# Kernel tuning notes

Hardware: AMD Instinct MI355X
Metric: run time of the kernel (lower is better)

## Reference

```python
import jax, jax.numpy as jnp
import numpy as np

EPS = 1e-08

def setup_inputs() -> dict:
    key = jax.random.key(0)
    k1, k2, k3, k4 = jax.random.split(key, 4)
    B, N, IN, OUT, WF = 16, 4096, 512, 512, 512
    x = jax.random.normal(k1, (B, N, IN), dtype=jnp.float32)
    w = jax.random.normal(k2, (B, WF), dtype=jnp.float32)
    # kaiming-normal-like init for the main weight
    weight = jax.random.normal(k3, (OUT, IN), dtype=jnp.float32) * np.sqrt(2.0 / IN)
    bias = jnp.zeros((OUT,), dtype=jnp.float32)
    A_w = jax.random.normal(k4, (IN, WF), dtype=jnp.float32) * np.sqrt(1.0 / WF)
    A_b = jnp.zeros((IN,), dtype=jnp.float32)
    return {"x": x, "w": w, "weight": weight, "bias": bias, "A_w": A_w, "A_b": A_b}

def reference(x, w, weight, bias, A_w, A_b):
    # style -> per-input-channel scale: (B, in)
    s = w @ A_w.T + A_b
    # modulate: (B, out, in)
    wm = weight[None, :, :] * s[:, None, :]
    # demodulate: rsqrt over in-dim
    norm = jax.lax.rsqrt(EPS + jnp.sum(wm * wm, axis=2, keepdims=True))
    wd = wm * norm
    # batched matmul: (B, N, in) x (B, out, in) -> (B, N, out)
    out = jnp.einsum('bni,boi->bno', x, wd) + bias
    return jax.nn.relu(out)
```

## Files before the change

kernel.cpp:

```cpp
#include <hip/hip_runtime.h>
#include <hip/hip_bf16.h>

#define B_    16
#define M_    4096
#define K_    512
#define O_    512

#define BM 128
#define BN 128
#define BK 32

typedef float f32x4 __attribute__((ext_vector_type(4)));
typedef short bf16x8 __attribute__((ext_vector_type(8)));
typedef unsigned short u16x8 __attribute__((ext_vector_type(8)));

__device__ __forceinline__ int chunk_off(int row, int kq) {
    return (row * 4 + (kq ^ ((row >> 1) & 3))) * 8;
}

__global__ void style_kernel(const float* __restrict__ w, const float* __restrict__ A_w,
                             const float* __restrict__ A_b, float* __restrict__ s) {
    int b = blockIdx.x;
    int i = blockIdx.y * 64 + threadIdx.x;
    __shared__ float wsh[512];
    for (int j = threadIdx.x; j < 512; j += 64) wsh[j] = w[b * 512 + j];
    __syncthreads();
    const float* arow = A_w + (size_t)i * 512;
    float acc = 0.f;
    #pragma unroll 4
    for (int f = 0; f < 512; f += 4) {
        float4 a = *(const float4*)(arow + f);
        acc += a.x * wsh[f] + a.y * wsh[f + 1] + a.z * wsh[f + 2] + a.w * wsh[f + 3];
    }
    s[b * 512 + i] = acc + A_b[i];
}

__global__ void demod_kernel(const float* __restrict__ weight, const float* __restrict__ s,
                             unsigned short* __restrict__ wd) {
    int gw = blockIdx.x * 4 + (threadIdx.x >> 6);
    int lane = threadIdx.x & 63;
    int b = gw >> 9;
    int o = gw & 511;
    const float* wrow = weight + (size_t)o * 512;
    const float* srow = s + b * 512;
    float vals[8];
    float ss = 0.f;
    #pragma unroll
    for (int j = 0; j < 8; j++) {
        int i = lane + j * 64;
        float v = wrow[i] * srow[i];
        vals[j] = v;
        ss += v * v;
    }
    #pragma unroll
    for (int off = 32; off; off >>= 1) ss += __shfl_xor(ss, off);
    float nrm = rsqrtf(1e-8f + ss);
    unsigned short* drow = wd + ((size_t)b * 512 + o) * 512;
    #pragma unroll
    for (int j = 0; j < 8; j++) {
        int i = lane + j * 64;
        unsigned int u = __builtin_bit_cast(unsigned int, vals[j] * nrm);
        u += 0x7fffu + ((u >> 16) & 1u);
        drow[i] = (unsigned short)(u >> 16);
    }
}

__global__ __launch_bounds__(256, 3) void gemm_kernel(const float* __restrict__ x,
                                                      const unsigned short* __restrict__ wd,
                                                      const float* __restrict__ bias,
                                                      float* __restrict__ out) {
    __shared__ unsigned short sA[2][BM * BK];
    __shared__ unsigned short sB[2][BN * BK];

    int g = blockIdx.x;
    int xcd = g & 7;
    int grp = g >> 3;
    int nblk = grp & 3;
    int mb = xcd * 64 + (grp >> 2);
    const int b  = mb >> 5;
    const int m0 = (mb & 31) * BM;
    const int n0 = nblk * BN;

    const float* xb = x + (size_t)b * M_ * K_;
    const unsigned short* wdb = wd + (size_t)b * O_ * K_;

    const int t = threadIdx.x;
    const int w = t >> 6;
    const int l = t & 63;
    const int wave_row = (w >> 1) * 64;
    const int wave_col = (w & 1) * 64;
    const int lrow  = l & 15;
    const int kq_l  = l >> 4;

    int offA[4], offB[4];
    #pragma unroll
    for (int mi = 0; mi < 4; mi++)
        offA[mi] = chunk_off(wave_row + mi * 16 + lrow, kq_l);
    #pragma unroll
    for (int ni = 0; ni < 4; ni++)
        offB[ni] = chunk_off(wave_col + ni * 16 + lrow, kq_l);

    const int ar = t >> 1;
    const int akq0 = (t & 1) * 2;
    const float* abase = xb + (size_t)(m0 + ar) * K_ + akq0 * 8;

    int bchunk[2], brow[2], bkq[2];
    #pragma unroll
    for (int j = 0; j < 2; j++) {
        int c = w * 128 + j * 64 + l;
        brow[j] = c >> 2;
        bkq[j] = (c & 3) ^ ((brow[j] >> 1) & 3);
        bchunk[j] = c;
    }

    f32x4 acc[4][4] = {};
    f32x4 areg[4];

    #pragma unroll
    for (int j = 0; j < 2; j++) {
        __builtin_amdgcn_global_load_lds(
            (const __attribute__((address_space(1))) unsigned int*)(wdb + (size_t)(n0 + brow[j]) * K_ + bkq[j] * 8),
            (__attribute__((address_space(3))) unsigned int*)(&sB[0][bchunk[j] * 8]),
            16, 0, 0);
    }
    #pragma unroll
    for (int j = 0; j < 4; j++) areg[j] = *(const f32x4*)(abase + j * 4);
    #pragma unroll
    for (int j = 0; j < 2; j++) {
        union { __hip_bfloat162 h[4]; u16x8 v; } cv;
        cv.h[0] = __float22bfloat162_rn(float2{areg[2*j][0], areg[2*j][1]});
        cv.h[1] = __float22bfloat162_rn(float2{areg[2*j][2], areg[2*j][3]});
        cv.h[2] = __float22bfloat162_rn(float2{areg[2*j+1][0], areg[2*j+1][1]});
        cv.h[3] = __float22bfloat162_rn(float2{areg[2*j+1][2], areg[2*j+1][3]});
        *(u16x8*)(&sA[0][chunk_off(ar, akq0 + j)]) = cv.v;
    }
    __syncthreads();

    int cur = 0;
    #pragma unroll 2
    for (int kk = 0; kk < K_; kk += BK) {
        int nxt = cur ^ 1;
        bool pf = (kk + BK) < K_;
        if (pf) {
            #pragma unroll
            for (int j = 0; j < 2; j++) {
                __builtin_amdgcn_global_load_lds(
                    (const __attribute__((address_space(1))) unsigned int*)(wdb + (size_t)(n0 + brow[j]) * K_ + kk + BK + bkq[j] * 8),
                    (__attribute__((address_space(3))) unsigned int*)(&sB[nxt][bchunk[j] * 8]),
                    16, 0, 0);
            }
            #pragma unroll
            for (int j = 0; j < 4; j++) areg[j] = *(const f32x4*)(abase + kk + BK + j * 4);
        }

        bf16x8 af[4], bfr[4];
        #pragma unroll
        for (int mi = 0; mi < 4; mi++) af[mi] = *(const bf16x8*)(&sA[cur][offA[mi]]);
        #pragma unroll
        for (int ni = 0; ni < 4; ni++) bfr[ni] = *(const bf16x8*)(&sB[cur][offB[ni]]);
        #pragma unroll
        for (int mi = 0; mi < 4; mi++)
            #pragma unroll
            for (int ni = 0; ni < 4; ni++)
                acc[mi][ni] = __builtin_amdgcn_mfma_f32_16x16x32_bf16(af[mi], bfr[ni], acc[mi][ni], 0, 0, 0);

        if (pf) {
            #pragma unroll
            for (int j = 0; j < 2; j++) {
                union { __hip_bfloat162 h[4]; u16x8 v; } cv;
                cv.h[0] = __float22bfloat162_rn(float2{areg[2*j][0], areg[2*j][1]});
                cv.h[1] = __float22bfloat162_rn(float2{areg[2*j][2], areg[2*j][3]});
                cv.h[2] = __float22bfloat162_rn(float2{areg[2*j+1][0], areg[2*j+1][1]});
                cv.h[3] = __float22bfloat162_rn(float2{areg[2*j+1][2], areg[2*j+1][3]});
                *(u16x8*)(&sA[nxt][chunk_off(ar, akq0 + j)]) = cv.v;
            }
        }
        __syncthreads();
        cur = nxt;
    }

    const int col_l = l & 15;
    const int row_q = (l >> 4) * 4;
    #pragma unroll
    for (int ni = 0; ni < 4; ni++) {
        int o = n0 + wave_col + ni * 16 + col_l;
        float bv = bias[o];
        #pragma unroll
        for (int mi = 0; mi < 4; mi++) {
            int mrow = m0 + wave_row + mi * 16 + row_q;
            #pragma unroll
            for (int r = 0; r < 4; r++) {
                float v = acc[mi][ni][r] + bv;
                out[((size_t)b * M_ + mrow + r) * O_ + o] = v > 0.f ? v : 0.f;
            }
        }
    }
}

extern "C" void kernel_launch(void* const* d_in, const int* in_sizes, int n_in,
                              void* d_out, int out_size, void* d_ws, size_t ws_size,
                              hipStream_t stream) {
    const float* x      = (const float*)d_in[0];
    const float* w      = (const float*)d_in[1];
    const float* weight = (const float*)d_in[2];
    const float* bias   = (const float*)d_in[3];
    const float* A_w    = (const float*)d_in[4];
    const float* A_b    = (const float*)d_in[5];
    float* out = (float*)d_out;

    unsigned short* wd = (unsigned short*)d_ws;
    float* s = (float*)((char*)d_ws + (size_t)B_ * O_ * K_ * sizeof(unsigned short));

    style_kernel<<<dim3(B_, 8), 64, 0, stream>>>(w, A_w, A_b, s);
    demod_kernel<<<(B_ * O_) / 4, 256, 0, stream>>>(weight, s, wd);
    gemm_kernel<<<2048, 256, 0, stream>>>(x, wd, bias, out);
}
```

Measured before the change: 308.1 us.

## Deepen GEMM pipeline to triple-buffered LDS with two-tile-ahead prefetch

Moves the GEMM main loop from double to triple-buffered LDS and issues global loads two k-tiles ahead, alternating two register sets for the fp32 A tile. Plain __syncthreads is replaced by explicit s_waitcnt vmcnt(6) plus a barrier, so the next tile's loads can stay in flight while the current tile is computed. The aim is to hide global memory latency better. In exchange it uses more LDS (48KB per block, which may limit residency at 3 blocks per CU) and more registers, and correctness depends on the hand-counted vmcnt value.

```diff
diff --git a/kernel.cpp b/kernel.cpp
--- a/kernel.cpp
+++ b/kernel.cpp
@@ -9,6 +9,7 @@
 #define BM 128
 #define BN 128
 #define BK 32
+#define NT (K_ / BK)
 
 typedef float f32x4 __attribute__((ext_vector_type(4)));
 typedef short bf16x8 __attribute__((ext_vector_type(8)));
@@ -65,12 +66,63 @@
     }
 }
 
+
+#define ISSUE_B(tile, buf)                                                              \
+    _Pragma("unroll")                                                                   \
+    for (int j = 0; j < 2; j++) {                                                       \
+        __builtin_amdgcn_global_load_lds(                                               \
+            (const __attribute__((address_space(1))) unsigned int*)(                    \
+                wdb + (size_t)(n0 + brow[j]) * K_ + (tile) * BK + bkq[j] * 8),          \
+            (__attribute__((address_space(3))) unsigned int*)(&sB[buf][bchunk[j] * 8]), \
+            16, 0, 0);                                                                  \
+    }
+
+#define LOAD_A(tile, regs)                                                              \
+    _Pragma("unroll")                                                                   \
+    for (int j = 0; j < 4; j++) regs[j] = *(const f32x4*)(abase + (tile) * BK + j * 4);
+
+#define CVT_A(regs, buf)                                                                \
+    _Pragma("unroll")                                                                   \
+    for (int j = 0; j < 2; j++) {                                                       \
+        union { __hip_bfloat162 h[4]; u16x8 v; } cv;                                    \
+        cv.h[0] = __float22bfloat162_rn(float2{regs[2*j][0], regs[2*j][1]});            \
+        cv.h[1] = __float22bfloat162_rn(float2{regs[2*j][2], regs[2*j][3]});            \
+        cv.h[2] = __float22bfloat162_rn(float2{regs[2*j+1][0], regs[2*j+1][1]});        \
+        cv.h[3] = __float22bfloat162_rn(float2{regs[2*j+1][2], regs[2*j+1][3]});        \
+        *(u16x8*)(&sA[buf][chunk_off(ar, akq0 + j)]) = cv.v;                            \
+    }
+
+#define COMPUTE(buf)                                                                    \
+    {                                                                                   \
+        bf16x8 af[4], bfr[4];                                                           \
+        _Pragma("unroll")                                                               \
+        for (int mi = 0; mi < 4; mi++) af[mi] = *(const bf16x8*)(&sA[buf][offA[mi]]);   \
+        _Pragma("unroll")                                                               \
+        for (int ni = 0; ni < 4; ni++) bfr[ni] = *(const bf16x8*)(&sB[buf][offB[ni]]);  \
+        _Pragma("unroll")                                                               \
+        for (int mi = 0; mi < 4; mi++)                                                  \
+            _Pragma("unroll")                                                           \
+            for (int ni = 0; ni < 4; ni++)                                              \
+                acc[mi][ni] = __builtin_amdgcn_mfma_f32_16x16x32_bf16(                  \
+                    af[mi], bfr[ni], acc[mi][ni], 0, 0, 0);                             \
+    }
+
+#define FENCE6() do {                                                                   \
+    asm volatile("s_waitcnt vmcnt(6) lgkmcnt(0)" ::: "memory");                         \
+    __builtin_amdgcn_s_barrier();                                                       \
+} while (0)
+
+#define FENCE0() do {                                                                   \
+    asm volatile("s_waitcnt vmcnt(0) lgkmcnt(0)" ::: "memory");                         \
+    __builtin_amdgcn_s_barrier();                                                       \
+} while (0)
+
 __global__ __launch_bounds__(256, 3) void gemm_kernel(const float* __restrict__ x,
                                                       const unsigned short* __restrict__ wd,
                                                       const float* __restrict__ bias,
                                                       float* __restrict__ out) {
-    __shared__ unsigned short sA[2][BM * BK];
-    __shared__ unsigned short sB[2][BN * BK];
+    __shared__ unsigned short sA[3][BM * BK];
+    __shared__ unsigned short sB[3][BN * BK];
 
     int g = blockIdx.x;
     int xcd = g & 7;
@@ -114,69 +166,29 @@
     }
 
     f32x4 acc[4][4] = {};
-    f32x4 areg[4];
-
-    #pragma unroll
-    for (int j = 0; j < 2; j++) {
-        __builtin_amdgcn_global_load_lds(
-            (const __attribute__((address_space(1))) unsigned int*)(wdb + (size_t)(n0 + brow[j]) * K_ + bkq[j] * 8),
-            (__attribute__((address_space(3))) unsigned int*)(&sB[0][bchunk[j] * 8]),
-            16, 0, 0);
-    }
-    #pragma unroll
-    for (int j = 0; j < 4; j++) areg[j] = *(const f32x4*)(abase + j * 4);
-    #pragma unroll
-    for (int j = 0; j < 2; j++) {
-        union { __hip_bfloat162 h[4]; u16x8 v; } cv;
-        cv.h[0] = __float22bfloat162_rn(float2{areg[2*j][0], areg[2*j][1]});
-        cv.h[1] = __float22bfloat162_rn(float2{areg[2*j][2], areg[2*j][3]});
-        cv.h[2] = __float22bfloat162_rn(float2{areg[2*j+1][0], areg[2*j+1][1]});
-        cv.h[3] = __float22bfloat162_rn(float2{areg[2*j+1][2], areg[2*j+1][3]});
-        *(u16x8*)(&sA[0][chunk_off(ar, akq0 + j)]) = cv.v;
-    }
-    __syncthreads();
-
-    int cur = 0;
-    #pragma unroll 2
-    for (int kk = 0; kk < K_; kk += BK) {
-        int nxt = cur ^ 1;
-        bool pf = (kk + BK) < K_;
-        if (pf) {
-            #pragma unroll
-            for (int j = 0; j < 2; j++) {
-                __builtin_amdgcn_global_load_lds(
-                    (const __attribute__((address_space(1))) unsigned int*)(wdb + (size_t)(n0 + brow[j]) * K_ + kk + BK + bkq[j] * 8),
-                    (__attribute__((address_space(3))) unsigned int*)(&sB[nxt][bchunk[j] * 8]),
-                    16, 0, 0);
-            }
-            #pragma unroll
-            for (int j = 0; j < 4; j++) areg[j] = *(const f32x4*)(abase + kk + BK + j * 4);
+    f32x4 areg0[4], areg1[4];
+
+    ISSUE_B(0, 0);
+    LOAD_A(0, areg0);
+    asm volatile("" ::: "memory");
+    ISSUE_B(1, 1);
+    LOAD_A(1, areg1);
+    CVT_A(areg0, 0);
+    FENCE6();
+
+    #pragma unroll
+    for (int k = 0; k < NT; k++) {
+        if (k + 2 < NT) {
+            ISSUE_B(k + 2, (k + 2) % 3);
+            if ((k & 1) == 0) { LOAD_A(k + 2, areg0); } else { LOAD_A(k + 2, areg1); }
         }
 
-        bf16x8 af[4], bfr[4];
-        #pragma unroll
-        for (int mi = 0; mi < 4; mi++) af[mi] = *(const bf16x8*)(&sA[cur][offA[mi]]);
-        #pragma unroll
-        for (int ni = 0; ni < 4; ni++) bfr[ni] = *(const bf16x8*)(&sB[cur][offB[ni]]);
-        #pragma unroll
-        for (int mi = 0; mi < 4; mi++)
-            #pragma unroll
-            for (int ni = 0; ni < 4; ni++)
-                acc[mi][ni] = __builtin_amdgcn_mfma_f32_16x16x32_bf16(af[mi], bfr[ni], acc[mi][ni], 0, 0, 0);
-
-        if (pf) {
-            #pragma unroll
-            for (int j = 0; j < 2; j++) {
-                union { __hip_bfloat162 h[4]; u16x8 v; } cv;
-                cv.h[0] = __float22bfloat162_rn(float2{areg[2*j][0], areg[2*j][1]});
-                cv.h[1] = __float22bfloat162_rn(float2{areg[2*j][2], areg[2*j][3]});
-                cv.h[2] = __float22bfloat162_rn(float2{areg[2*j+1][0], areg[2*j+1][1]});
-                cv.h[3] = __float22bfloat162_rn(float2{areg[2*j+1][2], areg[2*j+1][3]});
-                *(u16x8*)(&sA[nxt][chunk_off(ar, akq0 + j)]) = cv.v;
-            }
+        COMPUTE(k % 3);
+
+        if (k + 1 < NT) {
+            if ((k & 1) == 0) { CVT_A(areg1, (k + 1) % 3); } else { CVT_A(areg0, (k + 1) % 3); }
+            if (k + 2 < NT) { FENCE6(); } else { FENCE0(); }
         }
-        __syncthreads();
-        cur = nxt;
     }
 
     const int col_l = l & 15;
```

Measured after the change: 340.9 us. 10.6% more time.

## Restructure GEMM: full-K A tile in LDS, B fragments loaded directly from pre-swizzled layout

Applied to the files above, without the earlier changes.

The demod kernel now writes the modulated weights in an MFMA-fragment-ordered layout, so the GEMM can load B fragments straight from global memory into registers with double buffering and no LDS staging. Each GEMM block covers 64 rows and all 512 output columns, loading the whole 64x512 bf16 A tile into LDS once. This removes the per-k-step barriers and uses setprio around the MFMA burst. The style kernel is rebuilt to compute 16 outputs per block from LDS-staged tiles. In exchange, register pressure is higher (128 accumulator vectors plus 16 B fragments per wave), occupancy is capped at 2 blocks, and there are fewer blocks.

```diff
diff --git a/kernel.cpp b/kernel.cpp
--- a/kernel.cpp
+++ b/kernel.cpp
@@ -6,192 +6,155 @@
 #define K_    512
 #define O_    512
 
-#define BM 128
-#define BN 128
-#define BK 32
+#define BM 64
+#define NT 16
 
 typedef float f32x4 __attribute__((ext_vector_type(4)));
 typedef short bf16x8 __attribute__((ext_vector_type(8)));
 typedef unsigned short u16x8 __attribute__((ext_vector_type(8)));
 
-__device__ __forceinline__ int chunk_off(int row, int kq) {
-    return (row * 4 + (kq ^ ((row >> 1) & 3))) * 8;
-}
-
 __global__ void style_kernel(const float* __restrict__ w, const float* __restrict__ A_w,
                              const float* __restrict__ A_b, float* __restrict__ s) {
-    int b = blockIdx.x;
-    int i = blockIdx.y * 64 + threadIdx.x;
-    __shared__ float wsh[512];
-    for (int j = threadIdx.x; j < 512; j += 64) wsh[j] = w[b * 512 + j];
+    __shared__ float wsh[16][516];
+    __shared__ float ash[16][516];
+    int t = threadIdx.x;
+    for (int idx = t; idx < 2048; idx += 256) {
+        int row = idx >> 7, q = (idx & 127) * 4;
+        *(float4*)&wsh[row][q] = *(const float4*)&w[row * 512 + q];
+    }
+    int i0 = blockIdx.x * 16;
+    for (int idx = t; idx < 2048; idx += 256) {
+        int row = idx >> 7, q = (idx & 127) * 4;
+        *(float4*)&ash[row][q] = *(const float4*)&A_w[(size_t)(i0 + row) * 512 + q];
+    }
     __syncthreads();
-    const float* arow = A_w + (size_t)i * 512;
+    int b = t >> 4, il = t & 15;
     float acc = 0.f;
-    #pragma unroll 4
+    #pragma unroll 8
     for (int f = 0; f < 512; f += 4) {
-        float4 a = *(const float4*)(arow + f);
-        acc += a.x * wsh[f] + a.y * wsh[f + 1] + a.z * wsh[f + 2] + a.w * wsh[f + 3];
+        float4 wa = *(const float4*)&wsh[b][f];
+        float4 aa = *(const float4*)&ash[il][f];
+        acc += wa.x * aa.x + wa.y * aa.y + wa.z * aa.z + wa.w * aa.w;
     }
-    s[b * 512 + i] = acc + A_b[i];
+    s[b * 512 + i0 + il] = acc + A_b[i0 + il];
 }
 
 __global__ void demod_kernel(const float* __restrict__ weight, const float* __restrict__ s,
-                             unsigned short* __restrict__ wd) {
+                             unsigned short* __restrict__ wd2) {
     int gw = blockIdx.x * 4 + (threadIdx.x >> 6);
     int lane = threadIdx.x & 63;
     int b = gw >> 9;
     int o = gw & 511;
     const float* wrow = weight + (size_t)o * 512;
     const float* srow = s + b * 512;
+    int k0 = lane * 8;
+    f32x4 w0 = *(const f32x4*)(wrow + k0);
+    f32x4 w1 = *(const f32x4*)(wrow + k0 + 4);
+    f32x4 s0 = *(const f32x4*)(srow + k0);
+    f32x4 s1 = *(const f32x4*)(srow + k0 + 4);
     float vals[8];
     float ss = 0.f;
     #pragma unroll
-    for (int j = 0; j < 8; j++) {
-        int i = lane + j * 64;
-        float v = wrow[i] * srow[i];
-        vals[j] = v;
-        ss += v * v;
-    }
+    for (int j = 0; j < 4; j++) { float v = w0[j] * s0[j]; vals[j] = v; ss += v * v; }
+    #pragma unroll
+    for (int j = 0; j < 4; j++) { float v = w1[j] * s1[j]; vals[4 + j] = v; ss += v * v; }
     #pragma unroll
     for (int off = 32; off; off >>= 1) ss += __shfl_xor(ss, off);
     float nrm = rsqrtf(1e-8f + ss);
-    unsigned short* drow = wd + ((size_t)b * 512 + o) * 512;
+    int ks = lane >> 2, kq = lane & 3;
+    size_t base = (((((size_t)b * 16 + ks) * 32 + (o >> 4)) * 4 + kq) * 16 + (o & 15)) * 8;
+    u16x8 pack;
     #pragma unroll
     for (int j = 0; j < 8; j++) {
-        int i = lane + j * 64;
         unsigned int u = __builtin_bit_cast(unsigned int, vals[j] * nrm);
         u += 0x7fffu + ((u >> 16) & 1u);
-        drow[i] = (unsigned short)(u >> 16);
+        pack[j] = (unsigned short)(u >> 16);
     }
+    *(u16x8*)(wd2 + base) = pack;
 }
 
-__global__ __launch_bounds__(256, 3) void gemm_kernel(const float* __restrict__ x,
-                                                      const unsigned short* __restrict__ wd,
+__global__ __launch_bounds__(256, 2) void gemm_kernel(const float* __restrict__ x,
+                                                      const unsigned short* __restrict__ wd2,
                                                       const float* __restrict__ bias,
                                                       float* __restrict__ out) {
-    __shared__ unsigned short sA[2][BM * BK];
-    __shared__ unsigned short sB[2][BN * BK];
+    __shared__ unsigned short sA[BM * 64 * 8];
 
     int g = blockIdx.x;
     int xcd = g & 7;
-    int grp = g >> 3;
-    int nblk = grp & 3;
-    int mb = xcd * 64 + (grp >> 2);
-    const int b  = mb >> 5;
-    const int m0 = (mb & 31) * BM;
-    const int n0 = nblk * BN;
-
-    const float* xb = x + (size_t)b * M_ * K_;
-    const unsigned short* wdb = wd + (size_t)b * O_ * K_;
+    int r = g >> 3;
+    const int b  = xcd * 2 + (r >> 6);
+    const int m0 = (r & 63) * BM;
 
     const int t = threadIdx.x;
     const int w = t >> 6;
     const int l = t & 63;
-    const int wave_row = (w >> 1) * 64;
-    const int wave_col = (w & 1) * 64;
-    const int lrow  = l & 15;
-    const int kq_l  = l >> 4;
 
-    int offA[4], offB[4];
+    const float* xb = x + ((size_t)b * M_ + m0) * K_;
     #pragma unroll
-    for (int mi = 0; mi < 4; mi++)
-        offA[mi] = chunk_off(wave_row + mi * 16 + lrow, kq_l);
-    #pragma unroll
-    for (int ni = 0; ni < 4; ni++)
-        offB[ni] = chunk_off(wave_col + ni * 16 + lrow, kq_l);
-
-    const int ar = t >> 1;
-    const int akq0 = (t & 1) * 2;
-    const float* abase = xb + (size_t)(m0 + ar) * K_ + akq0 * 8;
-
-    int bchunk[2], brow[2], bkq[2];
-    #pragma unroll
-    for (int j = 0; j < 2; j++) {
-        int c = w * 128 + j * 64 + l;
-        brow[j] = c >> 2;
-        bkq[j] = (c & 3) ^ ((brow[j] >> 1) & 3);
-        bchunk[j] = c;
-    }
-
-    f32x4 acc[4][4] = {};
-    f32x4 areg[4];
-
-    #pragma unroll
-    for (int j = 0; j < 2; j++) {
-        __builtin_amdgcn_global_load_lds(
-            (const __attribute__((address_space(1))) unsigned int*)(wdb + (size_t)(n0 + brow[j]) * K_ + bkq[j] * 8),
-            (__attribute__((address_space(3))) unsigned int*)(&sB[0][bchunk[j] * 8]),
-            16, 0, 0);
-    }
-    #pragma unroll
-    for (int j = 0; j < 4; j++) areg[j] = *(const f32x4*)(abase + j * 4);
-    #pragma unroll
-    for (int j = 0; j < 2; j++) {
-        union { __hip_bfloat162 h[4]; u16x8 v; } cv;
-        cv.h[0] = __float22bfloat162_rn(float2{areg[2*j][0], areg[2*j][1]});
-        cv.h[1] = __float22bfloat162_rn(float2{areg[2*j][2], areg[2*j][3]});
-        cv.h[2] = __float22bfloat162_rn(float2{areg[2*j+1][0], areg[2*j+1][1]});
-        cv.h[3] = __float22bfloat162_rn(float2{areg[2*j+1][2], areg[2*j+1][3]});
-        *(u16x8*)(&sA[0][chunk_off(ar, akq0 + j)]) = cv.v;
+    for (int rr = 0; rr < 16; rr++) {
+        int row = rr * 4 + w;
+        const float* src = xb + (size_t)row * K_ + l * 8;
+        f32x4 u = *(const f32x4*)src;
+        f32x4 v = *(const f32x4*)(src + 4);
+        union { __hip_bfloat162 h[4]; u16x8 vv; } cv;
+        cv.h[0] = __float22bfloat162_rn(float2{u[0], u[1]});
+        cv.h[1] = __float22bfloat162_rn(float2{u[2], u[3]});
+        cv.h[2] = __float22bfloat162_rn(float2{v[0], v[1]});
+        cv.h[3] = __float22bfloat162_rn(float2{v[2], v[3]});
+        int chunk = row * 64 + (l & ~7) + ((l ^ row) & 7);
+        *(u16x8*)(&sA[chunk * 8]) = cv.vv;
     }
     __syncthreads();
 
-    int cur = 0;
-    #pragma unroll 2
-    for (int kk = 0; kk < K_; kk += BK) {
-        int nxt = cur ^ 1;
-        bool pf = (kk + BK) < K_;
-        if (pf) {
+    const unsigned short* wb = wd2 + (size_t)b * 262144 + (size_t)(w * 8) * 512 + (size_t)l * 8;
+
+    const int rowl = l & 15;
+    const int kqv  = l >> 4;
+
+    f32x4 acc[4][8] = {};
+    bf16x8 bfr[2][8];
+
+    #pragma unroll
+    for (int ni = 0; ni < 8; ni++)
+        bfr[0][ni] = *(const bf16x8*)(wb + (size_t)ni * 512);
+
+    #pragma unroll
+    for (int ks = 0; ks < NT; ks++) {
+        if (ks + 1 < NT) {
             #pragma unroll
-            for (int j = 0; j < 2; j++) {
-                __builtin_amdgcn_global_load_lds(
-                    (const __attribute__((address_space(1))) unsigned int*)(wdb + (size_t)(n0 + brow[j]) * K_ + kk + BK + bkq[j] * 8),
-                    (__attribute__((address_space(3))) unsigned int*)(&sB[nxt][bchunk[j] * 8]),
-                    16, 0, 0);
-            }
-            #pragma unroll
-            for (int j = 0; j < 4; j++) areg[j] = *(const f32x4*)(abase + kk + BK + j * 4);
+            for (int ni = 0; ni < 8; ni++)
+                bfr[(ks + 1) & 1][ni] = *(const bf16x8*)(wb + ((size_t)(ks + 1) * 32 + ni) * 512);
         }
-
-        bf16x8 af[4], bfr[4];
+        bf16x8 af[4];
         #pragma unroll
-        for (int mi = 0; mi < 4; mi++) af[mi] = *(const bf16x8*)(&sA[cur][offA[mi]]);
-        #pragma unroll
-        for (int ni = 0; ni < 4; ni++) bfr[ni] = *(const bf16x8*)(&sB[cur][offB[ni]]);
+        for (int mi = 0; mi < 4; mi++) {
+            int row = mi * 16 + rowl;
+            int c = ks * 4 + kqv;
+            int chunk = row * 64 + (c & ~7) + ((c ^ row) & 7);
+            af[mi] = *(const bf16x8*)(&sA[chunk * 8]);
+        }
+        __builtin_amdgcn_s_setprio(1);
         #pragma unroll
         for (int mi = 0; mi < 4; mi++)
             #pragma unroll
-            for (int ni = 0; ni < 4; ni++)
-                acc[mi][ni] = __builtin_amdgcn_mfma_f32_16x16x32_bf16(af[mi], bfr[ni], acc[mi][ni], 0, 0, 0);
-
-        if (pf) {
-            #pragma unroll
-            for (int j = 0; j < 2; j++) {
-                union { __hip_bfloat162 h[4]; u16x8 v; } cv;
-                cv.h[0] = __float22bfloat162_rn(float2{areg[2*j][0], areg[2*j][1]});
-                cv.h[1] = __float22bfloat162_rn(float2{areg[2*j][2], areg[2*j][3]});
-                cv.h[2] = __float22bfloat162_rn(float2{areg[2*j+1][0], areg[2*j+1][1]});
-                cv.h[3] = __float22bfloat162_rn(float2{areg[2*j+1][2], areg[2*j+1][3]});
-                *(u16x8*)(&sA[nxt][chunk_off(ar, akq0 + j)]) = cv.v;
-            }
-        }
-        __syncthreads();
-        cur = nxt;
+            for (int ni = 0; ni < 8; ni++)
+                acc[mi][ni] = __builtin_amdgcn_mfma_f32_16x16x32_bf16(af[mi], bfr[ks & 1][ni], acc[mi][ni], 0, 0, 0);
+        __builtin_amdgcn_s_setprio(0);
     }
 
     const int col_l = l & 15;
     const int row_q = (l >> 4) * 4;
     #pragma unroll
-    for (int ni = 0; ni < 4; ni++) {
-        int o = n0 + wave_col + ni * 16 + col_l;
+    for (int ni = 0; ni < 8; ni++) {
+        int o = w * 128 + ni * 16 + col_l;
         float bv = bias[o];
         #pragma unroll
         for (int mi = 0; mi < 4; mi++) {
-            int mrow = m0 + wave_row + mi * 16 + row_q;
+            int mrow = m0 + mi * 16 + row_q;
             #pragma unroll
-            for (int r = 0; r < 4; r++) {
-                float v = acc[mi][ni][r] + bv;
-                out[((size_t)b * M_ + mrow + r) * O_ + o] = v > 0.f ? v : 0.f;
+            for (int rr2 = 0; rr2 < 4; rr2++) {
+                float v = acc[mi][ni][rr2] + bv;
+                out[((size_t)b * M_ + mrow + rr2) * O_ + o] = v > 0.f ? v : 0.f;
             }
         }
     }
@@ -208,10 +171,10 @@
     const float* A_b    = (const float*)d_in[5];
     float* out = (float*)d_out;
 
-    unsigned short* wd = (unsigned short*)d_ws;
+    unsigned short* wd2 = (unsigned short*)d_ws;
     float* s = (float*)((char*)d_ws + (size_t)B_ * O_ * K_ * sizeof(unsigned short));
 
-    style_kernel<<<dim3(B_, 8), 64, 0, stream>>>(w, A_w, A_b, s);
-    demod_kernel<<<(B_ * O_) / 4, 256, 0, stream>>>(weight, s, wd);
-    gemm_kernel<<<2048, 256, 0, stream>>>(x, wd, bias, out);
+    style_kernel<<<32, 256, 0, stream>>>(w, A_w, A_b, s);
+    demod_kernel<<<(B_ * O_) / 4, 256, 0, stream>>>(weight, s, wd2);
+    gemm_kernel<<<1024, 256, 0, stream>>>(x, wd2, bias, out);
 }
```

After: 273.9 us. 11.1% less time.
